# Kernel optimization log

Hardware: AMD Instinct MI355X
Metric: run time of the kernel (lower is better)

The kernel has to match this reference:

```python
import jax, jax.numpy as jnp
import numpy as np

E = 128          # out_embedding_size
N = 128          # n_atoms
B = 512          # batch
CUTOFF = 5.0
LOG_STD_MIN, LOG_STD_MAX = -20.0, 2.0


def shifted_softplus(x):
    return jax.nn.softplus(x) - jnp.log(2.0).astype(x.dtype)


def cosine_cutoff(r):
    # SchNetPack CosineCutoff: 0.5*(cos(pi*r/rc)+1) for r < rc, else 0
    return 0.5 * (jnp.cos(r * (jnp.pi / CUTOFF)) + 1.0) * (r < CUTOFF).astype(r.dtype)


def setup_inputs() -> dict:
    key = jax.random.key(0)
    ks = jax.random.split(key, 8)
    kx = jax.random.normal(ks[0], (B, N, 2 * E + 1), dtype=jnp.float32)
    positions = jax.random.uniform(ks[1], (B, N, 3), dtype=jnp.float32) * 10.0
    # prefix-ones atoms mask (molecules padded at the end), 64..128 real atoms
    num_atoms = jax.random.randint(ks[2], (B,), 64, N + 1)
    atoms_mask = (jnp.arange(N)[None, :] < num_atoms[:, None]).astype(jnp.float32)
    eval_actions = jax.random.normal(ks[3], (B, N, 3), dtype=jnp.float32) * 0.1
    Wx = jax.random.normal(ks[4], (E, E), dtype=jnp.float32) / np.sqrt(E)
    bx = jnp.zeros((E,), dtype=jnp.float32)
    Wk = jax.random.normal(ks[5], (E, E), dtype=jnp.float32) / np.sqrt(E)
    bk = jnp.zeros((E,), dtype=jnp.float32)
    return {
        "kx": kx, "positions": positions, "atoms_mask": atoms_mask,
        "action_scale": jnp.float32(1.0), "eval_actions": eval_actions,
        "Wx": Wx, "bx": bx, "Wk": Wk, "bk": bk,
    }


def reference(kx, positions, atoms_mask, action_scale, eval_actions, Wx, bx, Wk, bk):
    kx = kx * atoms_mask[..., None]
    # P[b,i,j] = pos[b,j] - pos[b,i]
    P = positions[:, None, :, :] - positions[:, :, None, :]
    # safe norm: tiny eps inside sqrt so grads are finite on the zero diagonal
    r_ij = jnp.sqrt(jnp.sum(P * P, axis=-1) + 1e-16)
    P = P / (r_ij[..., None] + 1e-8)

    x = kx[..., :E]
    k = kx[..., E:2 * E]
    actions_log_std = kx[..., 2 * E:]  # [B,N,1]

    x = shifted_softplus(x) @ Wx.T + bx
    k = jax.nn.relu(k) @ Wk.T + bk

    inv_sqrt_e = 1.0 / jnp.sqrt(jnp.float32(E))
    x = jnp.einsum('bie,bje->bij', x, x) * inv_sqrt_e
    x = (r_ij - x) * 0.5
    k = jnp.einsum('bie,bje->bij', k, k) * inv_sqrt_e
    f = x * k

    # neighborhood mask: first num_atoms rows/cols are 1 (vectorized get_nbh_mask)
    counts = jnp.sum(atoms_mask, axis=-1)              # [B]
    idx = jnp.arange(N, dtype=counts.dtype)
    valid = (idx[None, :] < counts[:, None]).astype(f.dtype)   # [B,N]
    nbh_mask = valid[:, :, None] * valid[:, None, :]           # [B,N,N]

    fcut = cosine_cutoff(r_ij) * nbh_mask
    # summation_order='to' -> sum over dim 1
    actions_mean = jnp.sum(P * (f * fcut)[..., None], axis=1)  # [B,N,3]

    # limit_actions: tanh renormalization
    actions_norm = jnp.sqrt(jnp.sum(actions_mean * actions_mean, axis=-1) + 1e-16) + 1e-8
    actions_mean = actions_mean / actions_norm[..., None] * jnp.tanh(actions_norm)[..., None]

    # training path with eval_actions supplied
    actions_log_std = jnp.clip(actions_log_std, LOG_STD_MIN, LOG_STD_MAX)
    mu = actions_mean * action_scale
    sigma = jnp.exp(actions_log_std) * action_scale   # [B,N,1], broadcasts
    actions = eval_actions
    log_prob = (-0.5 * jnp.square((actions - mu) / sigma)
                - jnp.log(sigma)
                - 0.5 * jnp.log(2.0 * jnp.pi))
    log_prob = log_prob * atoms_mask[..., None]
    log_prob = jnp.sum(log_prob, axis=(1, 2))[:, None]  # [B,1]

    actions = actions * atoms_mask[..., None]
    return actions, log_prob
```

## Files before the change

kernel.cpp:

```cpp
#include <hip/hip_runtime.h>
#include <math.h>

#define EDIM 128
#define NATOM 128
#define NBATCH 512
#define THREADS 512
#define ROWLEN 257

typedef __attribute__((ext_vector_type(8))) short bf16x8;
typedef __attribute__((ext_vector_type(4))) float f32x4;
typedef __attribute__((ext_vector_type(4))) unsigned short u16x4;

__device__ __forceinline__ unsigned short f2bf(float f) {
    unsigned u = __float_as_uint(f);
    u += 0x7FFFu + ((u >> 16) & 1u);
    return (unsigned short)(u >> 16);
}
__device__ __forceinline__ unsigned short cvt1(float x) {
    unsigned r;
    asm("v_cvt_pk_bf16_f32 %0, %1, %1" : "=v"(r) : "v"(x));
    return (unsigned short)r;
}
__device__ __forceinline__ unsigned cvt2(float a0, float a1) {
    unsigned r;
    asm("v_cvt_pk_bf16_f32 %0, %1, %2" : "=v"(r) : "v"(a0), "v"(a1));
    return r;
}
__device__ __forceinline__ float fast_ssp(float x) {
    return fmaxf(x, 0.f) + __logf(1.f + __expf(-fabsf(x))) - 0.69314718055994531f;
}
__device__ __forceinline__ int swzp(int row, int cbyte, int phase) {
    return row * 256 + ((cbyte ^ phase) ^ ((row & 7) << 4));
}

#define PH 0
#define QH 32768

__global__ void wcvt_kernel(const float* __restrict__ Wx,
                            const float* __restrict__ Wk,
                            unsigned short* __restrict__ ws) {
    int g = blockIdx.x * 256 + threadIdx.x;
    const float* src = (g < 16384) ? Wx : Wk;
    ws[g] = f2bf(src[g & 16383]);
}

__global__ void __launch_bounds__(THREADS, 4)
gen_actions_kernel(const float* __restrict__ kx,
                   const float* __restrict__ pos,
                   const float* __restrict__ mask,
                   const float* __restrict__ scale_ptr,
                   const float* __restrict__ evala,
                   const float* __restrict__ bx,
                   const float* __restrict__ bk,
                   const unsigned short* __restrict__ ws,
                   float* __restrict__ out)
{
    extern __shared__ char lds[];
    __shared__ f32x4 posQs[NATOM];
    __shared__ float amBs[NATOM * 3];
    __shared__ float redBs[2];
    __shared__ int   cntBs[2];

    const int b = blockIdx.x;
    const int t = threadIdx.x;
    const int lane = t & 63;
    const int w = t >> 6;
    const int wrb = w >> 2;
    const int wc = w & 3;
    const int l15 = lane & 15;
    const int l4  = lane >> 4;

    if (t < NATOM) {
        float m = mask[b * NATOM + t];
        unsigned long long bal = __ballot(m > 0.5f);
        if ((t & 63) == 0) cntBs[t >> 6] = __popcll(bal);
        const float* p = pos + ((size_t)b * NATOM + t) * 3;
        f32x4 q;
        q[0] = p[0]; q[1] = p[1]; q[2] = p[2];
        q[3] = kx[(size_t)b * (NATOM * ROWLEN) + t * ROWLEN + 2 * EDIM];
        posQs[t] = q;
    }
    if (t < NATOM * 3) amBs[t] = 0.f;

    {
        float mA = mask[b * NATOM + lane];
        float mB = mask[b * NATOM + 64 + lane];
        int cnt = __popcll(__ballot(mA > 0.5f)) + __popcll(__ballot(mB > 0.5f));
        const int cnt32 = (cnt + 31) & ~31;
        const float* kb = kx + (size_t)b * (NATOM * ROWLEN);
        #pragma unroll 4
        for (int rr2 = 0; rr2 < 16; ++rr2) {
            const int row = rr2 * 8 + w;
            if (row < cnt32) {
                const float* src = kb + row * ROWLEN;
                float x0 = src[2 * lane];
                float x1 = src[2 * lane + 1];
                float y0 = src[128 + 2 * lane];
                float y1 = src[128 + 2 * lane + 1];
                unsigned pa = cvt2(fast_ssp(x0), fast_ssp(x1));
                unsigned pc = cvt2(fmaxf(y0, 0.f), fmaxf(y1, 0.f));
                *(unsigned*)(lds + PH + swzp(row, 4 * lane, 0))  = pa;
                *(unsigned*)(lds + QH + swzp(row, 4 * lane, 64)) = pc;
            }
        }
    }
    __syncthreads();
    const int count = cntBs[0] + cntBs[1];

    const int n0 = wc * 32;
    const bool nact = (n0 < count);

    #define GEMM_MAT(MAT, PLANE, PHASE, WSOFF, BIAS)                                    \
    {                                                                                   \
        u16x4 pk[2][2][2];                                                              \
        if (nact) {                                                                     \
            const char* act = lds + PLANE;                                              \
            const unsigned short* WH = ws + WSOFF;                                      \
            f32x4 acc[2][2][2] = {};                                                    \
            for (int ks = 0; ks < 4; ++ks) {                                            \
                const int e0 = ks * 32 + l4 * 8;                                        \
                bf16x8 ah[2];                                                           \
                _Pragma("unroll")                                                       \
                for (int nf = 0; nf < 2; ++nf)                                          \
                    ah[nf] = *(const bf16x8*)(act + swzp(n0 + nf * 16 + l15, e0 * 2, PHASE)); \
                _Pragma("unroll")                                                       \
                for (int p = 0; p < 2; ++p) {                                           \
                    _Pragma("unroll")                                                   \
                    for (int mf = 0; mf < 2; ++mf) {                                    \
                        int orow = (wrb + 2 * p) * 32 + mf * 16 + l15;                  \
                        bf16x8 wh = *(const bf16x8*)(WH + orow * 128 + e0);             \
                        _Pragma("unroll")                                               \
                        for (int nf = 0; nf < 2; ++nf)                                  \
                            acc[p][mf][nf] = __builtin_amdgcn_mfma_f32_16x16x32_bf16(wh, ah[nf], acc[p][mf][nf], 0, 0, 0); \
                    }                                                                   \
                }                                                                       \
            }                                                                           \
            _Pragma("unroll")                                                           \
            for (int p = 0; p < 2; ++p)                                                 \
                _Pragma("unroll")                                                       \
                for (int mf = 0; mf < 2; ++mf) {                                        \
                    int ob = (wrb + 2 * p) * 32 + mf * 16 + l4 * 4;                     \
                    f32x4 b4 = *(const f32x4*)(BIAS + ob);                              \
                    _Pragma("unroll")                                                   \
                    for (int nf = 0; nf < 2; ++nf) {                                    \
                        u16x4 hs;                                                       \
                        _Pragma("unroll")                                               \
                        for (int r = 0; r < 4; ++r) hs[r] = cvt1(acc[p][mf][nf][r] + b4[r]); \
                        pk[p][mf][nf] = hs;                                             \
                    }                                                                   \
                }                                                                       \
        }                                                                               \
        __syncthreads();                      \
        if (nact) {                                                                     \
            _Pragma("unroll")                                                           \
            for (int p = 0; p < 2; ++p)                                                 \
                _Pragma("unroll")                                                       \
                for (int mf = 0; mf < 2; ++mf) {                                        \
                    int ob2 = ((wrb + 2 * p) * 32 + mf * 16 + l4 * 4) * 2;              \
                    _Pragma("unroll")                                                   \
                    for (int nf = 0; nf < 2; ++nf) {                                    \
                        int jrow = n0 + nf * 16 + l15;                                  \
                        *(u16x4*)(lds + PLANE + swzp(jrow, ob2, PHASE)) = pk[p][mf][nf]; \
                    }                                                                   \
                }                                                                       \
        }                                                                               \
    }

    GEMM_MAT(0, PH, 0,  0,     bx)
    GEMM_MAT(1, QH, 64, 16384, bk)
    __syncthreads();

    const int n0g = n0;
    if (n0g < count) {
        f32x4 gx[2][2][2] = {}, gk[2][2][2] = {};
        for (int ks = 0; ks < 4; ++ks) {
            const int e0b = (ks * 32 + l4 * 8) * 2;
            bf16x8 bX[2], bK[2];
            #pragma unroll
            for (int nf = 0; nf < 2; ++nf) {
                bX[nf] = *(const bf16x8*)(lds + PH + swzp(n0g + nf * 16 + l15, e0b, 0));
                bK[nf] = *(const bf16x8*)(lds + QH + swzp(n0g + nf * 16 + l15, e0b, 64));
            }
            #pragma unroll
            for (int p = 0; p < 2; ++p) {
                const int m0g = (wrb + 2 * p) * 32;
                if (m0g < count) {
                    #pragma unroll
                    for (int mf = 0; mf < 2; ++mf) {
                        int irow = m0g + mf * 16 + l15;
                        bf16x8 aX = *(const bf16x8*)(lds + PH + swzp(irow, e0b, 0));
                        bf16x8 aK = *(const bf16x8*)(lds + QH + swzp(irow, e0b, 64));
                        #pragma unroll
                        for (int nf = 0; nf < 2; ++nf) {
                            gx[p][mf][nf] = __builtin_amdgcn_mfma_f32_16x16x32_bf16(aX, bX[nf], gx[p][mf][nf], 0, 0, 0);
                            gk[p][mf][nf] = __builtin_amdgcn_mfma_f32_16x16x32_bf16(aK, bK[nf], gk[p][mf][nf], 0, 0, 0);
                        }
                    }
                }
            }
        }
        const float inv_e = 0.08838834764831845f;
        float am[2][3] = {};
        f32x4 pj4[2];
        bool jv[2];
        #pragma unroll
        for (int nf = 0; nf < 2; ++nf) {
            const int j = n0g + nf * 16 + l15;
            jv[nf] = (j < count);
            pj4[nf] = posQs[j];
        }
        #pragma unroll
        for (int p = 0; p < 2; ++p) {
            const int m0g = (wrb + 2 * p) * 32;
            if (m0g < count) {
                #pragma unroll
                for (int mf = 0; mf < 2; ++mf) {
                    #pragma unroll
                    for (int r = 0; r < 4; ++r) {
                        const int i = m0g + mf * 16 + l4 * 4 + r;
                        f32x4 pi4 = posQs[i];
                        const bool iv = (i < count);
                        #pragma unroll
                        for (int nf = 0; nf < 2; ++nf) {
                            float dx = pj4[nf][0] - pi4[0];
                            float dy = pj4[nf][1] - pi4[1];
                            float dz = pj4[nf][2] - pi4[2];
                            float r2 = fmaf(dx, dx, fmaf(dy, dy, dz * dz)) + 1e-16f;
                            float rr = __builtin_amdgcn_sqrtf(r2);
                            bool ok = jv[nf] && iv && (rr < 5.0f);
                            float fc = ok ? (0.5f * (__cosf(rr * 0.62831853071795865f) + 1.f)) : 0.f;
                            float xs = fmaf(gx[p][mf][nf][r], -0.044194173824159216f, rr * 0.5f);
                            float fv = xs * (gk[p][mf][nf][r] * inv_e) * fc;
                            float wgt = fv * __builtin_amdgcn_rcpf(rr + 1e-8f);
                            am[nf][0] = fmaf(dx, wgt, am[nf][0]);
                            am[nf][1] = fmaf(dy, wgt, am[nf][1]);
                            am[nf][2] = fmaf(dz, wgt, am[nf][2]);
                        }
                    }
                }
            }
        }
        #pragma unroll
        for (int nf = 0; nf < 2; ++nf) {
            float amx = am[nf][0], amy = am[nf][1], amz = am[nf][2];
            amx += __shfl_xor(amx, 16); amx += __shfl_xor(amx, 32);
            amy += __shfl_xor(amy, 16); amy += __shfl_xor(amy, 32);
            amz += __shfl_xor(amz, 16); amz += __shfl_xor(amz, 32);
            if (l4 == 0 && jv[nf]) {
                const int j = n0g + nf * 16 + l15;
                atomicAdd(&amBs[j * 3 + 0], amx);
                atomicAdd(&amBs[j * 3 + 1], amy);
                atomicAdd(&amBs[j * 3 + 2], amz);
            }
        }
    }
    __syncthreads();

    if (t < 96) {
        f32x4 ev4 = *(const f32x4*)(evala + (size_t)b * 384 + t * 4);
        f32x4 o4;
        #pragma unroll
        for (int c = 0; c < 4; ++c) {
            int atom = (t * 4 + c) / 3;
            o4[c] = (atom < count) ? ev4[c] : 0.f;
        }
        *(f32x4*)(out + (size_t)b * 384 + t * 4) = o4;
    }
    float lp = 0.f;
    if (t < NATOM && t < count) {
        const float* ev = evala + ((size_t)b * NATOM + t) * 3;
        float e0v = ev[0], e1v = ev[1], e2v = ev[2];
        float scale = scale_ptr[0];
        f32x4 q = posQs[t];
        float ax = amBs[t * 3 + 0], ay = amBs[t * 3 + 1], az = amBs[t * 3 + 2];
        float nrm = sqrtf(fmaf(ax, ax, fmaf(ay, ay, az * az)) + 1e-16f) + 1e-8f;
        float qe = __expf(-2.f * nrm);
        float th = (1.f - qe) / (1.f + qe);
        float sc = th / nrm * scale;
        float ls = fminf(fmaxf(q[3], -20.f), 2.f);
        float sig = __expf(ls) * scale;
        float sinv = 1.f / sig;
        float zx = (e0v - ax * sc) * sinv;
        float zy = (e1v - ay * sc) * sinv;
        float zz = (e2v - az * sc) * sinv;
        lp = -0.5f * (zx * zx + zy * zy + zz * zz) - 3.f * __logf(sig)
             - 3.f * 0.91893853320467274f;
    }
    #pragma unroll
    for (int off = 32; off > 0; off >>= 1) lp += __shfl_down(lp, off);
    if (t == 0)  redBs[0] = lp;
    if (t == 64) redBs[1] = lp;
    __syncthreads();
    if (t == 0) out[(size_t)NBATCH * NATOM * 3 + b] = redBs[0] + redBs[1];
}

extern "C" void kernel_launch(void* const* d_in, const int* in_sizes, int n_in,
                              void* d_out, int out_size, void* d_ws, size_t ws_size,
                              hipStream_t stream) {
    const float* kx    = (const float*)d_in[0];
    const float* pos   = (const float*)d_in[1];
    const float* mask  = (const float*)d_in[2];
    const float* scale = (const float*)d_in[3];
    const float* ev    = (const float*)d_in[4];
    const float* Wx    = (const float*)d_in[5];
    const float* bx    = (const float*)d_in[6];
    const float* Wk    = (const float*)d_in[7];
    const float* bk    = (const float*)d_in[8];
    float* out = (float*)d_out;
    unsigned short* ws = (unsigned short*)d_ws;

    hipLaunchKernelGGL(wcvt_kernel, dim3(128), dim3(256), 0, stream, Wx, Wk, ws);

    const size_t shbytes = 65536;
    (void)hipFuncSetAttribute((const void*)gen_actions_kernel,
                              hipFuncAttributeMaxDynamicSharedMemorySize,
                              (int)shbytes);
    hipLaunchKernelGGL(gen_actions_kernel, dim3(NBATCH), dim3(THREADS), shbytes, stream,
                       kx, pos, mask, scale, ev, bx, bk, ws, out);
}
```

Measured before the change: 53.72 us.

## Double block to 1024 threads with one 32x32 output tile per wave

Doubles the threads per block from 512 to 1024, so the 16 waves each own a single 32x32 tile of the 128x128 outputs instead of two. This applies to the weight GEMMs, the pairwise Gram GEMMs and the force accumulation. The Gram computation is split into separate X and K passes to cut live accumulator registers, and launch bounds now target 8 waves per SIMD. The aim is more waves in flight and fewer registers per thread. In exchange, barriers cover more waves, LDS atomics contend more, and some waves sit idle when the atom count is small.

```diff
diff --git a/kernel.cpp b/kernel.cpp
--- a/kernel.cpp
+++ b/kernel.cpp
@@ -4,7 +4,7 @@
 #define EDIM 128
 #define NATOM 128
 #define NBATCH 512
-#define THREADS 512
+#define THREADS 1024
 #define ROWLEN 257
 
 typedef __attribute__((ext_vector_type(8))) short bf16x8;
@@ -44,7 +44,7 @@
     ws[g] = f2bf(src[g & 16383]);
 }
 
-__global__ void __launch_bounds__(THREADS, 4)
+__global__ void __launch_bounds__(THREADS, 8)
 gen_actions_kernel(const float* __restrict__ kx,
                    const float* __restrict__ pos,
                    const float* __restrict__ mask,
@@ -65,7 +65,7 @@
     const int t = threadIdx.x;
     const int lane = t & 63;
     const int w = t >> 6;
-    const int wrb = w >> 2;
+    const int wr = w >> 2;
     const int wc = w & 3;
     const int l15 = lane & 15;
     const int l4  = lane >> 4;
@@ -89,8 +89,8 @@
         const int cnt32 = (cnt + 31) & ~31;
         const float* kb = kx + (size_t)b * (NATOM * ROWLEN);
         #pragma unroll 4
-        for (int rr2 = 0; rr2 < 16; ++rr2) {
-            const int row = rr2 * 8 + w;
+        for (int r8 = 0; r8 < 8; ++r8) {
+            const int row = r8 * 16 + w;
             if (row < cnt32) {
                 const float* src = kb + row * ROWLEN;
                 float x0 = src[2 * lane];
@@ -107,16 +107,17 @@
     __syncthreads();
     const int count = cntBs[0] + cntBs[1];
 
+    const int m0 = wr * 32;
     const int n0 = wc * 32;
     const bool nact = (n0 < count);
 
-    #define GEMM_MAT(MAT, PLANE, PHASE, WSOFF, BIAS)                                    \
+    #define GEMM_MAT(PLANE, PHASE, WSOFF, BIAS)                                         \
     {                                                                                   \
-        u16x4 pk[2][2][2];                                                              \
+        u16x4 pk[2][2];                                                                 \
         if (nact) {                                                                     \
             const char* act = lds + PLANE;                                              \
             const unsigned short* WH = ws + WSOFF;                                      \
-            f32x4 acc[2][2][2] = {};                                                    \
+            f32x4 acc[2][2] = {};                                                       \
             for (int ks = 0; ks < 4; ++ks) {                                            \
                 const int e0 = ks * 32 + l4 * 8;                                        \
                 bf16x8 ah[2];                                                           \
@@ -124,79 +125,75 @@
                 for (int nf = 0; nf < 2; ++nf)                                          \
                     ah[nf] = *(const bf16x8*)(act + swzp(n0 + nf * 16 + l15, e0 * 2, PHASE)); \
                 _Pragma("unroll")                                                       \
-                for (int p = 0; p < 2; ++p) {                                           \
+                for (int mf = 0; mf < 2; ++mf) {                                        \
+                    int orow = m0 + mf * 16 + l15;                                      \
+                    bf16x8 wh = *(const bf16x8*)(WH + orow * 128 + e0);                 \
                     _Pragma("unroll")                                                   \
-                    for (int mf = 0; mf < 2; ++mf) {                                    \
-                        int orow = (wrb + 2 * p) * 32 + mf * 16 + l15;                  \
-                        bf16x8 wh = *(const bf16x8*)(WH + orow * 128 + e0);             \
-                        _Pragma("unroll")                                               \
-                        for (int nf = 0; nf < 2; ++nf)                                  \
-                            acc[p][mf][nf] = __builtin_amdgcn_mfma_f32_16x16x32_bf16(wh, ah[nf], acc[p][mf][nf], 0, 0, 0); \
-                    }                                                                   \
+                    for (int nf = 0; nf < 2; ++nf)                                      \
+                        acc[mf][nf] = __builtin_amdgcn_mfma_f32_16x16x32_bf16(wh, ah[nf], acc[mf][nf], 0, 0, 0); \
                 }                                                                       \
             }                                                                           \
             _Pragma("unroll")                                                           \
-            for (int p = 0; p < 2; ++p)                                                 \
+            for (int mf = 0; mf < 2; ++mf) {                                            \
+                int ob = m0 + mf * 16 + l4 * 4;                                         \
+                f32x4 b4 = *(const f32x4*)(BIAS + ob);                                  \
                 _Pragma("unroll")                                                       \
-                for (int mf = 0; mf < 2; ++mf) {                                        \
-                    int ob = (wrb + 2 * p) * 32 + mf * 16 + l4 * 4;                     \
-                    f32x4 b4 = *(const f32x4*)(BIAS + ob);                              \
+                for (int nf = 0; nf < 2; ++nf) {                                        \
+                    u16x4 hs;                                                           \
                     _Pragma("unroll")                                                   \
-                    for (int nf = 0; nf < 2; ++nf) {                                    \
-                        u16x4 hs;                                                       \
-                        _Pragma("unroll")                                               \
-                        for (int r = 0; r < 4; ++r) hs[r] = cvt1(acc[p][mf][nf][r] + b4[r]); \
-                        pk[p][mf][nf] = hs;                                             \
-                    }                                                                   \
+                    for (int r = 0; r < 4; ++r) hs[r] = cvt1(acc[mf][nf][r] + b4[r]);   \
+                    pk[mf][nf] = hs;                                                    \
                 }                                                                       \
+            }                                                                           \
         }                                                                               \
         __syncthreads();                      \
         if (nact) {                                                                     \
             _Pragma("unroll")                                                           \
-            for (int p = 0; p < 2; ++p)                                                 \
+            for (int mf = 0; mf < 2; ++mf) {                                            \
+                int ob2 = (m0 + mf * 16 + l4 * 4) * 2;                                  \
                 _Pragma("unroll")                                                       \
-                for (int mf = 0; mf < 2; ++mf) {                                        \
-                    int ob2 = ((wrb + 2 * p) * 32 + mf * 16 + l4 * 4) * 2;              \
-                    _Pragma("unroll")                                                   \
-                    for (int nf = 0; nf < 2; ++nf) {                                    \
-                        int jrow = n0 + nf * 16 + l15;                                  \
-                        *(u16x4*)(lds + PLANE + swzp(jrow, ob2, PHASE)) = pk[p][mf][nf]; \
-                    }                                                                   \
+                for (int nf = 0; nf < 2; ++nf) {                                        \
+                    int jrow = n0 + nf * 16 + l15;                                      \
+                    *(u16x4*)(lds + PLANE + swzp(jrow, ob2, PHASE)) = pk[mf][nf];       \
                 }                                                                       \
+            }                                                                           \
         }                                                                               \
     }
 
-    GEMM_MAT(0, PH, 0,  0,     bx)
-    GEMM_MAT(1, QH, 64, 16384, bk)
+    GEMM_MAT(PH, 0,  0,     bx)
+    GEMM_MAT(QH, 64, 16384, bk)
     __syncthreads();
 
-    const int n0g = n0;
-    if (n0g < count) {
-        f32x4 gx[2][2][2] = {}, gk[2][2][2] = {};
+    const bool active = (m0 < count) && nact;
+    if (active) {
+        f32x4 gx[2][2] = {};
         for (int ks = 0; ks < 4; ++ks) {
             const int e0b = (ks * 32 + l4 * 8) * 2;
-            bf16x8 bX[2], bK[2];
-            #pragma unroll
-            for (int nf = 0; nf < 2; ++nf) {
-                bX[nf] = *(const bf16x8*)(lds + PH + swzp(n0g + nf * 16 + l15, e0b, 0));
-                bK[nf] = *(const bf16x8*)(lds + QH + swzp(n0g + nf * 16 + l15, e0b, 64));
-            }
-            #pragma unroll
-            for (int p = 0; p < 2; ++p) {
-                const int m0g = (wrb + 2 * p) * 32;
-                if (m0g < count) {
-                    #pragma unroll
-                    for (int mf = 0; mf < 2; ++mf) {
-                        int irow = m0g + mf * 16 + l15;
-                        bf16x8 aX = *(const bf16x8*)(lds + PH + swzp(irow, e0b, 0));
-                        bf16x8 aK = *(const bf16x8*)(lds + QH + swzp(irow, e0b, 64));
-                        #pragma unroll
-                        for (int nf = 0; nf < 2; ++nf) {
-                            gx[p][mf][nf] = __builtin_amdgcn_mfma_f32_16x16x32_bf16(aX, bX[nf], gx[p][mf][nf], 0, 0, 0);
-                            gk[p][mf][nf] = __builtin_amdgcn_mfma_f32_16x16x32_bf16(aK, bK[nf], gk[p][mf][nf], 0, 0, 0);
-                        }
-                    }
-                }
+            bf16x8 bX[2];
+            #pragma unroll
+            for (int nf = 0; nf < 2; ++nf)
+                bX[nf] = *(const bf16x8*)(lds + PH + swzp(n0 + nf * 16 + l15, e0b, 0));
+            #pragma unroll
+            for (int mf = 0; mf < 2; ++mf) {
+                bf16x8 aX = *(const bf16x8*)(lds + PH + swzp(m0 + mf * 16 + l15, e0b, 0));
+                #pragma unroll
+                for (int nf = 0; nf < 2; ++nf)
+                    gx[mf][nf] = __builtin_amdgcn_mfma_f32_16x16x32_bf16(aX, bX[nf], gx[mf][nf], 0, 0, 0);
+            }
+        }
+        f32x4 gk[2][2] = {};
+        for (int ks = 0; ks < 4; ++ks) {
+            const int e0b = (ks * 32 + l4 * 8) * 2;
+            bf16x8 bK[2];
+            #pragma unroll
+            for (int nf = 0; nf < 2; ++nf)
+                bK[nf] = *(const bf16x8*)(lds + QH + swzp(n0 + nf * 16 + l15, e0b, 64));
+            #pragma unroll
+            for (int mf = 0; mf < 2; ++mf) {
+                bf16x8 aK = *(const bf16x8*)(lds + QH + swzp(m0 + mf * 16 + l15, e0b, 64));
+                #pragma unroll
+                for (int nf = 0; nf < 2; ++nf)
+                    gk[mf][nf] = __builtin_amdgcn_mfma_f32_16x16x32_bf16(aK, bK[nf], gk[mf][nf], 0, 0, 0);
             }
         }
         const float inv_e = 0.08838834764831845f;
@@ -205,38 +202,32 @@
         bool jv[2];
         #pragma unroll
         for (int nf = 0; nf < 2; ++nf) {
-            const int j = n0g + nf * 16 + l15;
+            const int j = n0 + nf * 16 + l15;
             jv[nf] = (j < count);
             pj4[nf] = posQs[j];
         }
         #pragma unroll
-        for (int p = 0; p < 2; ++p) {
-            const int m0g = (wrb + 2 * p) * 32;
-            if (m0g < count) {
+        for (int mf = 0; mf < 2; ++mf) {
+            #pragma unroll
+            for (int r = 0; r < 4; ++r) {
+                const int i = m0 + mf * 16 + l4 * 4 + r;
+                f32x4 pi4 = posQs[i];
+                const bool iv = (i < count);
                 #pragma unroll
-                for (int mf = 0; mf < 2; ++mf) {
-                    #pragma unroll
-                    for (int r = 0; r < 4; ++r) {
-                        const int i = m0g + mf * 16 + l4 * 4 + r;
-                        f32x4 pi4 = posQs[i];
-                        const bool iv = (i < count);
-                        #pragma unroll
-                        for (int nf = 0; nf < 2; ++nf) {
-                            float dx = pj4[nf][0] - pi4[0];
-                            float dy = pj4[nf][1] - pi4[1];
-                            float dz = pj4[nf][2] - pi4[2];
-                            float r2 = fmaf(dx, dx, fmaf(dy, dy, dz * dz)) + 1e-16f;
-                            float rr = __builtin_amdgcn_sqrtf(r2);
-                            bool ok = jv[nf] && iv && (rr < 5.0f);
-                            float fc = ok ? (0.5f * (__cosf(rr * 0.62831853071795865f) + 1.f)) : 0.f;
-                            float xs = fmaf(gx[p][mf][nf][r], -0.044194173824159216f, rr * 0.5f);
-                            float fv = xs * (gk[p][mf][nf][r] * inv_e) * fc;
-                            float wgt = fv * __builtin_amdgcn_rcpf(rr + 1e-8f);
-                            am[nf][0] = fmaf(dx, wgt, am[nf][0]);
-                            am[nf][1] = fmaf(dy, wgt, am[nf][1]);
-                            am[nf][2] = fmaf(dz, wgt, am[nf][2]);
-                        }
-                    }
+                for (int nf = 0; nf < 2; ++nf) {
+                    float dx = pj4[nf][0] - pi4[0];
+                    float dy = pj4[nf][1] - pi4[1];
+                    float dz = pj4[nf][2] - pi4[2];
+                    float r2 = fmaf(dx, dx, fmaf(dy, dy, dz * dz)) + 1e-16f;
+                    float rr = __builtin_amdgcn_sqrtf(r2);
+                    bool ok = jv[nf] && iv && (rr < 5.0f);
+                    float fc = ok ? (0.5f * (__cosf(rr * 0.62831853071795865f) + 1.f)) : 0.f;
+                    float xs = fmaf(gx[mf][nf][r], -0.044194173824159216f, rr * 0.5f);
+                    float fv = xs * (gk[mf][nf][r] * inv_e) * fc;
+                    float wgt = fv * __builtin_amdgcn_rcpf(rr + 1e-8f);
+                    am[nf][0] = fmaf(dx, wgt, am[nf][0]);
+                    am[nf][1] = fmaf(dy, wgt, am[nf][1]);
+                    am[nf][2] = fmaf(dz, wgt, am[nf][2]);
                 }
             }
         }
@@ -247,7 +238,7 @@
             amy += __shfl_xor(amy, 16); amy += __shfl_xor(amy, 32);
             amz += __shfl_xor(amz, 16); amz += __shfl_xor(amz, 32);
             if (l4 == 0 && jv[nf]) {
-                const int j = n0g + nf * 16 + l15;
+                const int j = n0 + nf * 16 + l15;
                 atomicAdd(&amBs[j * 3 + 0], amx);
                 atomicAdd(&amBs[j * 3 + 1], amy);
                 atomicAdd(&amBs[j * 3 + 2], amz);
```

Result: faster. 47.99 us, median of 2 (-10.7%).
